# Kernel optimization log

Measured on AMD Instinct MI355X. Metric: run time of the kernel, lower is better.

## Reference

```python
import jax, jax.numpy as jnp
import numpy as np

H = 16   # heads
DK = 64  # d_model // heads
LN_EPS = 1e-5


def setup_inputs() -> dict:
    key = jax.random.key(0)
    ks = jax.random.split(key, 6)
    bs, S, D = 2, 1024, 1024
    lim = 1.0 / np.sqrt(DK)  # torch Linear default init scale
    return {
        "context": jax.random.normal(ks[0], (bs, S, D), jnp.float32),
        "eos_mask": jnp.ones((bs, 1, S, S), jnp.bool_),
        "prior": jax.random.uniform(ks[1], (bs, H, S, S), jnp.float32),
        "ln_w": jnp.ones((D,), jnp.float32),
        "ln_b": jnp.zeros((D,), jnp.float32),
        "wk": jax.random.uniform(ks[2], (DK, DK), jnp.float32, -lim, lim),
        "bk": jax.random.uniform(ks[3], (DK,), jnp.float32, -lim, lim),
        "wq": jax.random.uniform(ks[4], (DK, DK), jnp.float32, -lim, lim),
        "bq": jax.random.uniform(ks[5], (DK,), jnp.float32, -lim, lim),
    }


def reference(context, eos_mask, prior, ln_w, ln_b, wk, bk, wq, bq):
    bs, S, D = context.shape
    # LayerNorm (torch uses biased variance)
    mu = context.mean(-1, keepdims=True)
    var = context.var(-1, keepdims=True)
    x = (context - mu) / jnp.sqrt(var + LN_EPS) * ln_w + ln_b
    # [bs, h, S, dk]
    x = x.reshape(bs, S, H, DK).transpose(0, 2, 1, 3)

    a = jnp.eye(S, k=1, dtype=jnp.float32)    # superdiagonal
    c = jnp.eye(S, k=-1, dtype=jnp.float32)   # subdiagonal
    eye = jnp.eye(S, dtype=jnp.float32)
    mask = eos_mask & ((a + c) > 0)           # [bs,1,S,S] tridiagonal (no diag)

    k = x @ wk.T + bk
    q = x @ wq.T + bq
    scores = jnp.einsum('bhqd,bhkd->bhqk', q, k) / DK
    scores = jnp.where(mask, scores, -10000.0)
    neibor = jax.nn.softmax(scores, axis=-1)
    # symmetrized geometric-mean neighbor attention
    neibor = jnp.sqrt(neibor * jnp.swapaxes(neibor, -2, -1) + 1e-4)
    neibor = prior + (1.0 - prior) * neibor

    tri = jnp.triu(jnp.ones((S, S), jnp.float32))  # incl. diag
    # keep log only on the superdiagonal, then prefix-sum via triu matmuls
    logn = jnp.where(a > 0, jnp.log(neibor + 1e-9), 0.0)
    t = logn @ tri                      # [bs,h,S,S]
    g = jnp.exp(jnp.matmul(tri, t))     # broadcasted [S,S] @ [bs,h,S,S]
    g = jnp.where((tri - eye) > 0, g, 0.0)  # keep strict upper triangle
    g = g + jnp.swapaxes(g, -2, -1) + jnp.where(eye > 0, neibor, 1e-4)
    return g, neibor


if __name__ == "__main__":
    out = reference(**setup_inputs())
    print(out[0].shape, out[1].shape)
```

## Files before the change

kernel.cpp:

```cpp
#include <hip/hip_runtime.h>
#include <hip/hip_bf16.h>

#define S 1024
#define H 16
#define BS 2
#define D 1024

__global__ __launch_bounds__(256) void k_ln_prep(const float* __restrict__ ctx,
                                                 const float* __restrict__ wk,
                                                 const float* __restrict__ bk,
                                                 const float* __restrict__ wq,
                                                 const float* __restrict__ bq,
                                                 float* __restrict__ mean,
                                                 float* __restrict__ rstd,
                                                 float* __restrict__ Mt,
                                                 float* __restrict__ uvec) {
    __shared__ float sh[2 * 64 * 65];
    int t = threadIdx.x;
    int bid = blockIdx.x;

    if (bid >= BS * S) {
        int p = bid - BS * S;
        float* WqL = sh;
        float* WkL = sh + 64 * 65;
        for (int idx = t; idx < 4096; idx += 256) {
            int d = idx >> 6, c = idx & 63;
            WqL[d * 65 + c] = wq[idx];
            WkL[d * 65 + c] = wk[idx];
        }
        __syncthreads();
        int a = t & 63, sub = t >> 6;
        for (int ee = sub; ee < 16; ee += 4) {
            int e = p * 16 + ee;
            float acc = 0.0f;
            #pragma unroll 8
            for (int d = 0; d < 64; ++d) acc += WqL[d * 65 + a] * WkL[d * 65 + e];
            Mt[e * 64 + a] = acc;
        }
        if (p == 0 && t < 64) {
            float acc = 0.0f;
            #pragma unroll 8
            for (int d = 0; d < 64; ++d) acc += bq[d] * WkL[d * 65 + t];
            uvec[t] = acc;
        }
        return;
    }

    const float* x = ctx + (size_t)bid * D;
    float4 v = *(const float4*)(x + t * 4);
    float s = v.x + v.y + v.z + v.w;
    float sq = v.x * v.x + v.y * v.y + v.z * v.z + v.w * v.w;
    #pragma unroll
    for (int off = 32; off > 0; off >>= 1) {
        s += __shfl_down(s, off);
        sq += __shfl_down(sq, off);
    }
    float* ss = sh;
    float* sqs = sh + 4;
    int w = t >> 6;
    if ((t & 63) == 0) { ss[w] = s; sqs[w] = sq; }
    __syncthreads();
    if (t == 0) {
        float sum = ss[0] + ss[1] + ss[2] + ss[3];
        float sumsq = sqs[0] + sqs[1] + sqs[2] + sqs[3];
        float m = sum * (1.0f / D);
        float var = sumsq * (1.0f / D) - m * m;
        mean[bid] = m;
        rstd[bid] = rsqrtf(var + 1e-5f);
    }
}

__global__ __launch_bounds__(256) void k_scores(const float* __restrict__ ctx,
                                                const float* __restrict__ mean,
                                                const float* __restrict__ rstd,
                                                const float* __restrict__ lnw,
                                                const float* __restrict__ lnb,
                                                const float* __restrict__ Mt,
                                                const float* __restrict__ uvec,
                                                float* __restrict__ p_up,
                                                float* __restrict__ p_dn) {
    int chunk = blockIdx.x;
    int bh = blockIdx.y;
    int b = bh >> 4, h = bh & 15;
    int r0 = chunk * 64;
    int t = threadIdx.x;

    __shared__ float xs[72][65];
    __shared__ float ts[72][65];
    __shared__ float Ml[64 * 64];
    __shared__ float ul[64];

    for (int idx = t; idx < 72 * 64; idx += 256) {
        int lr = idx >> 6, c = idx & 63;
        int row = r0 - 1 + lr;
        float v = 0.0f;
        if (lr < 66 && row >= 0 && row < S) {
            float cv = ctx[((size_t)b * S + row) * D + h * 64 + c];
            v = (cv - mean[b * S + row]) * rstd[b * S + row] * lnw[h * 64 + c] + lnb[h * 64 + c];
        }
        xs[lr][c] = v;
    }
    for (int idx = t; idx < 4096; idx += 256) Ml[idx] = Mt[idx];
    if (t < 64) ul[t] = uvec[t];
    __syncthreads();

    int a = t & 63, w = t >> 6;
    for (int s8 = w; s8 < 9; s8 += 4) {
        int rb = s8 * 8;
        float acc[8] = {0, 0, 0, 0, 0, 0, 0, 0};
        for (int e = 0; e < 64; ++e) {
            float m = Ml[e * 64 + a];
            #pragma unroll
            for (int rr = 0; rr < 8; ++rr)
                acc[rr] += xs[rb + rr][e] * m;
        }
        #pragma unroll
        for (int rr = 0; rr < 8; ++rr) ts[rb + rr][a] = acc[rr];
    }
    __syncthreads();

    if (t < 64) {
        int l = t;
        int i = r0 + l;
        float diff = 0.0f;
        #pragma unroll 4
        for (int d2 = 0; d2 < 64; ++d2) {
            float xi = xs[l + 1][d2];
            float tp = ts[l + 2][d2] - ts[l][d2];
            float xd = xs[l + 2][d2] - xs[l][d2];
            diff += xi * tp + ul[d2] * xd;
        }
        float z = diff * (1.0f / 64.0f);
        float pu, pd;
        if (i == 0)          { pu = 1.0f; pd = 0.0f; }
        else if (i == S - 1) { pu = 0.0f; pd = 1.0f; }
        else {
            float ez = __expf(-z);
            pu = 1.0f / (1.0f + ez);
            pd = 1.0f - pu;
        }
        p_up[bh * S + i] = pu;
        p_dn[bh * S + i] = pd;
    }
}

__global__ __launch_bounds__(1024) void k_scan(const float* __restrict__ p_up,
                                               const float* __restrict__ p_dn,
                                               const float* __restrict__ prior,
                                               float* __restrict__ n_up,
                                               float* __restrict__ C) {
    int bh = blockIdx.x;
    int t = threadIdx.x;
    float L = 0.0f;
    if (t > 0) {
        int i = t - 1;
        float nr = sqrtf(p_up[bh * S + i] * p_dn[bh * S + i + 1] + 1e-4f);
        n_up[bh * S + i] = nr;
        float pr = prior[((size_t)bh * S + i) * S + i + 1];
        float N = pr + (1.0f - pr) * nr;
        L = logf(N + 1e-9f);
    }
    int lane = t & 63, wid = t >> 6;
    float val = L;
    #pragma unroll
    for (int off = 1; off < 64; off <<= 1) {
        float v = __shfl_up(val, off, 64);
        if (lane >= off) val += v;
    }
    __shared__ float wsum[16];
    if (lane == 63) wsum[wid] = val;
    __syncthreads();
    if (t < 16) {
        float v2 = wsum[t];
        #pragma unroll
        for (int off = 1; off < 16; off <<= 1) {
            float x = __shfl_up(v2, off, 64);
            if (t >= off) v2 += x;
        }
        wsum[t] = v2;
    }
    __syncthreads();
    float base = (wid > 0) ? wsum[wid - 1] : 0.0f;
    C[bh * S + t] = base + val;
}

__global__ __launch_bounds__(256) void k_out(const float* __restrict__ prior,
                                             const float* __restrict__ n_up,
                                             const float* __restrict__ C,
                                             float* __restrict__ g_out,
                                             float* __restrict__ nb_out) {
    int bid = blockIdx.x;
    int bh = bid >> 10, i = bid & 1023;
    int t = threadIdx.x;
    size_t rowbase = (size_t)bid * S;
    float Ci = C[bh * S + i];
    float nup_i  = (i < S - 1) ? n_up[bh * S + i] : 0.0f;
    float nup_im = (i > 0)     ? n_up[bh * S + i - 1] : 0.0f;
    int j0 = t * 4;
    float4 p4 = *(const float4*)(prior + rowbase + j0);
    float4 c4 = *(const float4*)(C + bh * S + j0);
    float pv[4] = {p4.x, p4.y, p4.z, p4.w};
    float cv[4] = {c4.x, c4.y, c4.z, c4.w};
    float gv[4], nv[4];
    #pragma unroll
    for (int l = 0; l < 4; ++l) {
        int j = j0 + l;
        float p = pv[l];
        float v = 0.01f;
        if (j == i + 1) v = nup_i;
        if (j == i - 1) v = nup_im;
        float nb = p + (1.0f - p) * v;
        nv[l] = nb;
        float gg;
        if (j == i) {
            gg = nb;
        } else {
            float dd = (j > i) ? (cv[l] - Ci) : (Ci - cv[l]);
            gg = __expf(dd) + 1e-4f;
        }
        gv[l] = gg;
    }
    *(float4*)(g_out + rowbase + j0)  = make_float4(gv[0], gv[1], gv[2], gv[3]);
    *(float4*)(nb_out + rowbase + j0) = make_float4(nv[0], nv[1], nv[2], nv[3]);
}

extern "C" void kernel_launch(void* const* d_in, const int* in_sizes, int n_in,
                              void* d_out, int out_size, void* d_ws, size_t ws_size,
                              hipStream_t stream) {
    const float* ctx   = (const float*)d_in[0];
    const float* prior = (const float*)d_in[2];
    const float* lnw   = (const float*)d_in[3];
    const float* lnb   = (const float*)d_in[4];
    const float* wk    = (const float*)d_in[5];
    const float* bk    = (const float*)d_in[6];
    const float* wq    = (const float*)d_in[7];
    const float* bq    = (const float*)d_in[8];

    float* ws = (float*)d_ws;
    float* mean = ws;
    float* rstd = ws + 2048;
    float* Mt   = ws + 4096;
    float* uvec = ws + 8192;
    float* p_up = ws + 8448;
    float* p_dn = ws + 8448 + 32768;
    float* n_up = ws + 8448 + 65536;
    float* C    = ws + 8448 + 98304;

    float* g_out  = (float*)d_out;
    float* nb_out = (float*)d_out + (size_t)BS * H * S * S;

    k_ln_prep<<<BS * S + 4, 256, 0, stream>>>(ctx, wk, bk, wq, bq, mean, rstd, Mt, uvec);
    k_scores<<<dim3(16, BS * H), 256, 0, stream>>>(ctx, mean, rstd, lnw, lnb, Mt, uvec,
                                                   p_up, p_dn);
    k_scan<<<BS * H, 1024, 0, stream>>>(p_up, p_dn, prior, n_up, C);
    k_out<<<BS * H * S, 256, 0, stream>>>(prior, n_up, C, g_out, nb_out);
}
```

Before: 116.4 us.

## Register-resident weights and vectorized LDS in scores; nontemporal streaming in output kernel

The scores kernel now keeps each lane's column of the 64x64 combined weight matrix in registers instead of shared memory. It reads the normalized rows with float4 LDS loads using a padded stride of 68, and splits the per-row dot product across four lanes with a shuffle reduction, so all 256 threads take part instead of 64. The output kernel switches its prior load and both output stores to nontemporal builtins to avoid polluting cache on the large streaming traffic. The 64 extra registers per thread may reduce occupancy. The output kernel dominates runtime, so the nontemporal hints matter most.

```diff
diff --git a/kernel.cpp b/kernel.cpp
--- a/kernel.cpp
+++ b/kernel.cpp
@@ -5,6 +5,8 @@
 #define H 16
 #define BS 2
 #define D 1024
+
+typedef float f32x4 __attribute__((ext_vector_type(4)));
 
 __global__ __launch_bounds__(256) void k_ln_prep(const float* __restrict__ ctx,
                                                  const float* __restrict__ wk,
@@ -70,6 +72,7 @@
     }
 }
 
+#define XST 68
 __global__ __launch_bounds__(256) void k_scores(const float* __restrict__ ctx,
                                                 const float* __restrict__ mean,
                                                 const float* __restrict__ rstd,
@@ -84,11 +87,14 @@
     int b = bh >> 4, h = bh & 15;
     int r0 = chunk * 64;
     int t = threadIdx.x;
-
-    __shared__ float xs[72][65];
-    __shared__ float ts[72][65];
-    __shared__ float Ml[64 * 64];
-    __shared__ float ul[64];
+    int lane = t & 63, w = t >> 6;
+
+    __shared__ float xs[72][XST];
+    __shared__ float ts[72][XST];
+
+    float Mreg[64];
+    #pragma unroll
+    for (int e = 0; e < 64; ++e) Mreg[e] = Mt[e * 64 + lane];
 
     for (int idx = t; idx < 72 * 64; idx += 256) {
         int lr = idx >> 6, c = idx & 63;
@@ -100,47 +106,59 @@
         }
         xs[lr][c] = v;
     }
-    for (int idx = t; idx < 4096; idx += 256) Ml[idx] = Mt[idx];
-    if (t < 64) ul[t] = uvec[t];
-    __syncthreads();
-
-    int a = t & 63, w = t >> 6;
+    __syncthreads();
+
     for (int s8 = w; s8 < 9; s8 += 4) {
         int rb = s8 * 8;
         float acc[8] = {0, 0, 0, 0, 0, 0, 0, 0};
-        for (int e = 0; e < 64; ++e) {
-            float m = Ml[e * 64 + a];
+        #pragma unroll
+        for (int eq = 0; eq < 16; ++eq) {
             #pragma unroll
-            for (int rr = 0; rr < 8; ++rr)
-                acc[rr] += xs[rb + rr][e] * m;
-        }
-        #pragma unroll
-        for (int rr = 0; rr < 8; ++rr) ts[rb + rr][a] = acc[rr];
-    }
-    __syncthreads();
-
-    if (t < 64) {
-        int l = t;
-        int i = r0 + l;
+            for (int rr = 0; rr < 8; ++rr) {
+                float4 xv = *(const float4*)&xs[rb + rr][eq * 4];
+                acc[rr] += Mreg[eq * 4 + 0] * xv.x + Mreg[eq * 4 + 1] * xv.y +
+                           Mreg[eq * 4 + 2] * xv.z + Mreg[eq * 4 + 3] * xv.w;
+            }
+        }
+        #pragma unroll
+        for (int rr = 0; rr < 8; ++rr) ts[rb + rr][lane] = acc[rr];
+    }
+    __syncthreads();
+
+    {
+        int l = w * 16 + (lane >> 2);
+        int part = lane & 3;
         float diff = 0.0f;
-        #pragma unroll 4
-        for (int d2 = 0; d2 < 64; ++d2) {
-            float xi = xs[l + 1][d2];
-            float tp = ts[l + 2][d2] - ts[l][d2];
-            float xd = xs[l + 2][d2] - xs[l][d2];
-            diff += xi * tp + ul[d2] * xd;
-        }
-        float z = diff * (1.0f / 64.0f);
-        float pu, pd;
-        if (i == 0)          { pu = 1.0f; pd = 0.0f; }
-        else if (i == S - 1) { pu = 0.0f; pd = 1.0f; }
-        else {
-            float ez = __expf(-z);
-            pu = 1.0f / (1.0f + ez);
-            pd = 1.0f - pu;
-        }
-        p_up[bh * S + i] = pu;
-        p_dn[bh * S + i] = pd;
+        #pragma unroll
+        for (int dq = 0; dq < 4; ++dq) {
+            int d0 = part * 16 + dq * 4;
+            float4 xi = *(const float4*)&xs[l + 1][d0];
+            float4 t2 = *(const float4*)&ts[l + 2][d0];
+            float4 t0 = *(const float4*)&ts[l][d0];
+            float4 x2 = *(const float4*)&xs[l + 2][d0];
+            float4 x0 = *(const float4*)&xs[l][d0];
+            float4 uv = *(const float4*)&uvec[d0];
+            diff += xi.x * (t2.x - t0.x) + uv.x * (x2.x - x0.x);
+            diff += xi.y * (t2.y - t0.y) + uv.y * (x2.y - x0.y);
+            diff += xi.z * (t2.z - t0.z) + uv.z * (x2.z - x0.z);
+            diff += xi.w * (t2.w - t0.w) + uv.w * (x2.w - x0.w);
+        }
+        diff += __shfl_down(diff, 2);
+        diff += __shfl_down(diff, 1);
+        if (part == 0) {
+            int i = r0 + l;
+            float z = diff * (1.0f / 64.0f);
+            float pu, pd;
+            if (i == 0)          { pu = 1.0f; pd = 0.0f; }
+            else if (i == S - 1) { pu = 0.0f; pd = 1.0f; }
+            else {
+                float ez = __expf(-z);
+                pu = 1.0f / (1.0f + ez);
+                pd = 1.0f - pu;
+            }
+            p_up[bh * S + i] = pu;
+            p_dn[bh * S + i] = pd;
+        }
     }
 }
 
@@ -197,7 +215,7 @@
     float nup_i  = (i < S - 1) ? n_up[bh * S + i] : 0.0f;
     float nup_im = (i > 0)     ? n_up[bh * S + i - 1] : 0.0f;
     int j0 = t * 4;
-    float4 p4 = *(const float4*)(prior + rowbase + j0);
+    f32x4 p4 = __builtin_nontemporal_load((const f32x4*)(prior + rowbase + j0));
     float4 c4 = *(const float4*)(C + bh * S + j0);
     float pv[4] = {p4.x, p4.y, p4.z, p4.w};
     float cv[4] = {c4.x, c4.y, c4.z, c4.w};
@@ -220,8 +238,10 @@
         }
         gv[l] = gg;
     }
-    *(float4*)(g_out + rowbase + j0)  = make_float4(gv[0], gv[1], gv[2], gv[3]);
-    *(float4*)(nb_out + rowbase + j0) = make_float4(nv[0], nv[1], nv[2], nv[3]);
+    f32x4 gq = {gv[0], gv[1], gv[2], gv[3]};
+    f32x4 nq = {nv[0], nv[1], nv[2], nv[3]};
+    __builtin_nontemporal_store(gq, (f32x4*)(g_out + rowbase + j0));
+    __builtin_nontemporal_store(nq, (f32x4*)(nb_out + rowbase + j0));
 }
 
 extern "C" void kernel_launch(void* const* d_in, const int* in_sizes, int n_in,
```

Measured after the change: 106.0 us. -8.9%, faster.
